# Kernel tuning notes

Measured on AMD Instinct MI355X. Metric: run time of the kernel, lower is better.

## Reference

```python
import jax, jax.numpy as jnp
import numpy as np
from jax import lax

B, CIN, COUT, H, W, K = 32, 256, 256, 56, 56, 3

def setup_inputs() -> dict:
    key = jax.random.key(0)
    k1, k2, k3 = jax.random.split(key, 3)
    inp = jax.random.normal(k1, (B, CIN, H, W), dtype=jnp.float32)
    # kaiming-style init for conv kernel, normal init for bias
    fan_in = CIN * K * K
    kernel = jax.random.normal(k2, (COUT, CIN, K, K), dtype=jnp.float32) * np.float32(np.sqrt(2.0 / fan_in))
    bias = jax.random.normal(k3, (COUT,), dtype=jnp.float32)
    return {"inp": inp, "kernel": kernel, "bias": bias}

def reference(inp, kernel, bias):
    # Equivalent to the crossbar path: im2col 3x3 patches @ stacked [kernel|bias]
    # matrix == standard conv2d(padding=1, stride=1) + bias.
    out = lax.conv_general_dilated(
        inp, kernel,
        window_strides=(1, 1),
        padding=((1, 1), (1, 1)),
        dimension_numbers=("NCHW", "OIHW", "NCHW"),
    )
    return out + bias[None, :, None, None]
```

## Files before the change

kernel.cpp:

```cpp
#include <hip/hip_runtime.h>
#include <hip/hip_bf16.h>


#define BB    32
#define CINC  256
#define COUTC 256
#define HH    56
#define WW    56
#define HP    58
#define WP    58
#define PIX_PER_IMG 3136
#define NPIX  100352
#define KTOT  2304
#define NKT   72

#define XT_BYTES ((size_t)BB*HP*WP*CINC*2)
#define AWR_FRAGS (72*16*64)
#define AWR_BYTES ((size_t)AWR_FRAGS*16)

#define BUF_SZ 8192

using frag_t = __attribute__((ext_vector_type(8))) short;
using f32x4  = __attribute__((ext_vector_type(4))) float;

__device__ __forceinline__ void gload_lds16(const void* gsrc, void* ldst) {
  __builtin_amdgcn_global_load_lds(
      (const __attribute__((address_space(1))) unsigned*)gsrc,
      (__attribute__((address_space(3))) unsigned*)ldst, 16, 0, 0);
}

__global__ void xpose_kernel(const float* __restrict__ inp,
                             __hip_bfloat16* __restrict__ xt) {
  int bid = blockIdx.x;
  int hp = bid % HP;
  int t  = bid / HP;
  int cb = t % 4;
  int b  = t / 4;
  __shared__ __hip_bfloat16 tile[64 * 60];
  int tid = threadIdx.x;
  for (int i = tid; i < 64 * 60; i += 256) tile[i] = __float2bfloat16(0.f);
  __syncthreads();
  int h = hp - 1;
  if (h >= 0 && h < HH) {
    const float* src = inp + ((size_t)(b * CINC + cb * 64) * HH + h) * WW;
    for (int i = tid; i < 64 * WW; i += 256) {
      int ci = i / WW, w = i - ci * WW;
      tile[ci * 60 + (w + 1)] = __float2bfloat16(src[(size_t)ci * HH * WW + w]);
    }
  }
  __syncthreads();
  __hip_bfloat16* dst = xt + ((size_t)(b * HP + hp) * WP) * CINC + cb * 64;
  for (int i = tid; i < WP * 64; i += 256) {
    int wp = i >> 6, ci = i & 63;
    dst[(size_t)wp * CINC + ci] = tile[ci * 60 + wp];
  }
}

__global__ void wprep_pack(const float* __restrict__ k4,
                           frag_t* __restrict__ awr) {
  int i = blockIdx.x * 256 + threadIdx.x;
  if (i >= AWR_FRAGS) return;
  int lane = i & 63;
  int mb   = (i >> 6) & 15;
  int t    = i >> 10;
  int co   = mb * 16 + (lane & 15);
  int kb   = t * 32 + (lane >> 4) * 8;
  frag_t v;
#pragma unroll
  for (int j = 0; j < 8; ++j) {
    int k = kb + j;
    int tap = k >> 8;
    int ci  = k & 255;
    __hip_bfloat16 h = __float2bfloat16(k4[(co * CINC + ci) * 9 + tap]);
    v[j] = *reinterpret_cast<short*>(&h);
  }
  awr[i] = v;
}

__global__ __launch_bounds__(256, 2) void conv_areg(
    const __hip_bfloat16* __restrict__ xt,
    const frag_t* __restrict__ awr,
    const float* __restrict__ bias,
    float* __restrict__ out) {
  __shared__ alignas(16) char lds[3 * BUF_SZ];

  const int tid  = threadIdx.x;
  const int lane = tid & 63;
  const int wid  = tid >> 6;
  const int wm   = wid >> 1;
  const int wn   = wid & 1;
  const int fr   = lane & 15;
  const int g    = lane >> 4;

  const int bid   = blockIdx.x;
  const int ntile = (bid & 7) * 98 + (bid >> 3);

  const char* xt_b = (const char*)xt;

  const int lr  = lane >> 2;
  const int sc  = ((((lane & 3) - ((lane >> 3) & 3)) & 3) << 4);

  auto mkB = [&](int jb) -> const char* {
    int px = ntile * 128 + wid * 32 + jb * 16 + lr;
    int b  = px / PIX_PER_IMG;
    int hw = px - b * PIX_PER_IMG;
    int h = hw / WW, w = hw - h * WW;
    return xt_b + (size_t)((b * HP + h) * WP + w) * (CINC * 2) + sc;
  };
  const char* pB0 = mkB(0);
  const char* pB1 = mkB(1);

#define STG(T2, WB) {                                                      \
    int _tap = (T2) >> 3; int _rr = _tap / 3, _ss = _tap - _rr * 3;        \
    size_t _bo = (size_t)(_rr * WP + _ss) * (CINC * 2)                     \
               + (size_t)((T2) & 7) * 64;                                  \
    char* _d = lds + (WB) * BUF_SZ;                                        \
    gload_lds16(pB0 + _bo, _d + wid * 2048 + 0);                           \
    gload_lds16(pB1 + _bo, _d + wid * 2048 + 1024); }

  const frag_t* abase = awr + (size_t)(wm * 8) * 64 + lane;

#define ALOAD(T1, FA) {                                                    \
    const frag_t* _p = abase + (size_t)(T1) * (16 * 64);                   \
    _Pragma("unroll") for (int m = 0; m < 8; ++m)                          \
      FA[m] = _p[m * 64]; }

  const int ckr   = (((g + (fr >> 1)) & 3) << 4);
  const int broff = (wn * 64 + fr) * 64 + ckr;

  frag_t fa0[8], fa1[8], fb[4];
  f32x4 acc[8][4] = {};

#define RSL(RB) {                                                          \
    const char* _b = lds + (RB) * BUF_SZ;                                  \
    _Pragma("unroll") for (int n = 0; n < 4; ++n)                          \
      fb[n] = *(const frag_t*)(_b + broff + n * 1024); }

#define MF(FA) {                                                           \
    __builtin_amdgcn_s_setprio(1);                                         \
    _Pragma("unroll") for (int m = 0; m < 8; ++m)                          \
    _Pragma("unroll") for (int n = 0; n < 4; ++n)                          \
      acc[m][n] = __builtin_amdgcn_mfma_f32_16x16x32_bf16(                 \
          FA[m], fb[n], acc[m][n], 0, 0, 0);                               \
    __builtin_amdgcn_s_setprio(0); }

#define BODY(T, RB, WB, FCUR, FNXT) {                                      \
    STG((T) + 2, WB);                                                      \
    ALOAD((T) + 1, FNXT);                                                  \
    RSL(RB);                                                               \
    MF(FCUR);                                                              \
    asm volatile("s_waitcnt vmcnt(10)" ::: "memory");                      \
    __builtin_amdgcn_s_barrier();                                          \
    __builtin_amdgcn_sched_barrier(0); }

  STG(0, 0);
  STG(1, 1);
  ALOAD(0, fa0);
  asm volatile("s_waitcnt vmcnt(10)" ::: "memory");
  __builtin_amdgcn_s_barrier();
  __builtin_amdgcn_sched_barrier(0);

  for (int base = 0; base < 66; base += 6) {
    BODY(base + 0, 0, 2, fa0, fa1);
    BODY(base + 1, 1, 0, fa1, fa0);
    BODY(base + 2, 2, 1, fa0, fa1);
    BODY(base + 3, 0, 2, fa1, fa0);
    BODY(base + 4, 1, 0, fa0, fa1);
    BODY(base + 5, 2, 1, fa1, fa0);
  }
  BODY(66, 0, 2, fa0, fa1);
  BODY(67, 1, 0, fa1, fa0);
  BODY(68, 2, 1, fa0, fa1);
  BODY(69, 0, 2, fa1, fa0);

  {
    ALOAD(71, fa1);
    RSL(1);
    MF(fa0);
    asm volatile("s_waitcnt vmcnt(0)" ::: "memory");
    __builtin_amdgcn_s_barrier();
    __builtin_amdgcn_sched_barrier(0);
  }
  {
    RSL(2);
    MF(fa1);
  }

  int pb[4], phw[4];
#pragma unroll
  for (int n = 0; n < 4; ++n) {
    int pxg = ntile * 128 + wn * 64 + n * 16 + fr;
    pb[n]  = pxg / PIX_PER_IMG;
    phw[n] = pxg - pb[n] * PIX_PER_IMG;
  }
#pragma unroll
  for (int m = 0; m < 8; ++m) {
#pragma unroll
    for (int rg = 0; rg < 4; ++rg) {
      int co = wm * 128 + m * 16 + g * 4 + rg;
      float bv = bias[co];
#pragma unroll
      for (int n = 0; n < 4; ++n)
        out[((size_t)pb[n] * COUTC + co) * PIX_PER_IMG + phw[n]] =
            acc[m][n][rg] + bv;
    }
  }
}

__global__ void conv_direct(const float* __restrict__ inp,
                            const float* __restrict__ kern,
                            const float* __restrict__ bias,
                            float* __restrict__ out) {
  int idx = blockIdx.x * 256 + threadIdx.x;
  if (idx >= BB * COUTC * PIX_PER_IMG) return;
  int w = idx % WW;
  int t = idx / WW;
  int h = t % HH; t /= HH;
  int co = t % COUTC;
  int b  = t / COUTC;
  float acc = bias[co];
  for (int ci = 0; ci < CINC; ++ci)
    for (int r = 0; r < 3; ++r) {
      int hh = h + r - 1;
      if (hh < 0 || hh >= HH) continue;
      for (int s = 0; s < 3; ++s) {
        int ww2 = w + s - 1;
        if (ww2 < 0 || ww2 >= WW) continue;
        acc += inp[((size_t)(b * CINC + ci) * HH + hh) * WW + ww2] *
               kern[(co * CINC + ci) * 9 + r * 3 + s];
      }
    }
  out[idx] = acc;
}

extern "C" void kernel_launch(void* const* d_in, const int* in_sizes, int n_in,
                              void* d_out, int out_size, void* d_ws, size_t ws_size,
                              hipStream_t stream) {
  const float* inp  = (const float*)d_in[0];
  const float* kern = (const float*)d_in[1];
  const float* bias = (const float*)d_in[2];
  float* out = (float*)d_out;

  size_t need = XT_BYTES + AWR_BYTES;
  if (ws_size < need) {
    int tot = BB * COUTC * PIX_PER_IMG;
    conv_direct<<<(tot + 255) / 256, 256, 0, stream>>>(inp, kern, bias, out);
    return;
  }

  __hip_bfloat16* xt = (__hip_bfloat16*)d_ws;
  frag_t* awr = (frag_t*)((char*)d_ws + XT_BYTES);

  xpose_kernel<<<BB * 4 * HP, 256, 0, stream>>>(inp, xt);
  wprep_pack<<<(AWR_FRAGS + 255) / 256, 256, 0, stream>>>(kern, awr);
  conv_areg<<<NPIX / 128, 256, 0, stream>>>(xt, awr, bias, out);
}
```

Before: 185.5 us.

## Restructure conv GEMM into 512-thread 256x256 tiles with phased ping-pong pipeline

The implicit-GEMM conv kernel now uses 512-thread blocks, each computing a 256-cout by 256-pixel tile with 8 waves in a 2x4 arrangement. This replaces 256-thread blocks at two per CU. The K loop is split into half-tile phases: staging of B into four LDS buffers, A-register prefetch and MFMA groups are interleaved with barriers and explicit waitcnts, in a ping-pong schedule. The aim is better reuse per block and more overlap of global loads with MFMA work. In exchange it runs one block per CU with many more barriers, and the tail of the loop issues redundant clamped loads.

Measured after the change: 224.4 us. 1.21x slower.

```diff
diff --git a/kernel.cpp b/kernel.cpp
--- a/kernel.cpp
+++ b/kernel.cpp
@@ -18,7 +18,8 @@
 #define AWR_FRAGS (72*16*64)
 #define AWR_BYTES ((size_t)AWR_FRAGS*16)
 
-#define BUF_SZ 8192
+#define BUF_SZ 16384
+#define NT    392
 
 using frag_t = __attribute__((ext_vector_type(8))) short;
 using f32x4  = __attribute__((ext_vector_type(4))) float;
@@ -77,119 +78,128 @@
   awr[i] = v;
 }
 
-__global__ __launch_bounds__(256, 2) void conv_areg(
+__global__ __launch_bounds__(512, 1) void conv_ph(
     const __hip_bfloat16* __restrict__ xt,
     const frag_t* __restrict__ awr,
     const float* __restrict__ bias,
     float* __restrict__ out) {
-  __shared__ alignas(16) char lds[3 * BUF_SZ];
+  __shared__ alignas(16) char lds[4 * BUF_SZ];
 
   const int tid  = threadIdx.x;
   const int lane = tid & 63;
   const int wid  = tid >> 6;
-  const int wm   = wid >> 1;
-  const int wn   = wid & 1;
+  const int wm   = wid >> 2;
+  const int wn   = wid & 3;
   const int fr   = lane & 15;
   const int g    = lane >> 4;
 
   const int bid   = blockIdx.x;
-  const int ntile = (bid & 7) * 98 + (bid >> 3);
+  const int ptile = (bid & 7) * 49 + (bid >> 3);
 
   const char* xt_b = (const char*)xt;
 
   const int lr  = lane >> 2;
   const int sc  = ((((lane & 3) - ((lane >> 3) & 3)) & 3) << 4);
 
-  auto mkB = [&](int jb) -> const char* {
-    int px = ntile * 128 + wid * 32 + jb * 16 + lr;
+  auto mkB = [&](int h) -> const char* {
+    int px = ptile * 256 + h * 128 + wid * 16 + lr;
     int b  = px / PIX_PER_IMG;
     int hw = px - b * PIX_PER_IMG;
-    int h = hw / WW, w = hw - h * WW;
-    return xt_b + (size_t)((b * HP + h) * WP + w) * (CINC * 2) + sc;
+    int hh = hw / WW, w = hw - hh * WW;
+    return xt_b + (size_t)((b * HP + hh) * WP + w) * (CINC * 2) + sc;
   };
   const char* pB0 = mkB(0);
   const char* pB1 = mkB(1);
 
-#define STG(T2, WB) {                                                      \
-    int _tap = (T2) >> 3; int _rr = _tap / 3, _ss = _tap - _rr * 3;        \
+#define STG1(KT, WB, H) {                                                  \
+    int _kt = (KT) <= 71 ? (KT) : 71;                                      \
+    int _tap = _kt >> 3; int _rr = _tap / 3, _ss = _tap - _rr * 3;         \
     size_t _bo = (size_t)(_rr * WP + _ss) * (CINC * 2)                     \
-               + (size_t)((T2) & 7) * 64;                                  \
-    char* _d = lds + (WB) * BUF_SZ;                                        \
-    gload_lds16(pB0 + _bo, _d + wid * 2048 + 0);                           \
-    gload_lds16(pB1 + _bo, _d + wid * 2048 + 1024); }
+               + (size_t)(_kt & 7) * 64;                                   \
+    gload_lds16(((H) ? pB1 : pB0) + _bo,                                   \
+                lds + (WB) * BUF_SZ + (H) * 8192 + wid * 1024); }
 
   const frag_t* abase = awr + (size_t)(wm * 8) * 64 + lane;
 
-#define ALOAD(T1, FA) {                                                    \
-    const frag_t* _p = abase + (size_t)(T1) * (16 * 64);                   \
-    _Pragma("unroll") for (int m = 0; m < 8; ++m)                          \
-      FA[m] = _p[m * 64]; }
+#define ALOAD4(T1, QM, DST) {                                              \
+    int _t = (T1) <= 71 ? (T1) : 71;                                       \
+    const frag_t* _p = abase + ((size_t)_t * 16 + (QM) * 4) * 64;          \
+    _Pragma("unroll") for (int m = 0; m < 4; ++m)                          \
+      (DST)[m] = _p[m * 64]; }
 
   const int ckr   = (((g + (fr >> 1)) & 3) << 4);
   const int broff = (wn * 64 + fr) * 64 + ckr;
 
-  frag_t fa0[8], fa1[8], fb[4];
+  frag_t fa0[8], fa1[8], fbA[4], fbB[4];
   f32x4 acc[8][4] = {};
 
-#define RSL(RB) {                                                          \
+#define RSL(RB, FB) {                                                      \
     const char* _b = lds + (RB) * BUF_SZ;                                  \
     _Pragma("unroll") for (int n = 0; n < 4; ++n)                          \
-      fb[n] = *(const frag_t*)(_b + broff + n * 1024); }
-
-#define MF(FA) {                                                           \
-    __builtin_amdgcn_s_setprio(1);                                         \
-    _Pragma("unroll") for (int m = 0; m < 8; ++m)                          \
+      (FB)[n] = *(const frag_t*)(_b + broff + n * 1024); }
+
+#define MFP(QM, FA, FB) {                                                  \
+    __builtin_amdgcn_s_setprio(1);                                        \
+    _Pragma("unroll") for (int m = 0; m < 4; ++m)                          \
     _Pragma("unroll") for (int n = 0; n < 4; ++n)                          \
-      acc[m][n] = __builtin_amdgcn_mfma_f32_16x16x32_bf16(                 \
-          FA[m], fb[n], acc[m][n], 0, 0, 0);                               \
+      acc[(QM) * 4 + m][n] = __builtin_amdgcn_mfma_f32_16x16x32_bf16(      \
+          (FA)[(QM) * 4 + m], (FB)[n], acc[(QM) * 4 + m][n], 0, 0, 0);     \
     __builtin_amdgcn_s_setprio(0); }
 
-#define BODY(T, RB, WB, FCUR, FNXT) {                                      \
-    STG((T) + 2, WB);                                                      \
-    ALOAD((T) + 1, FNXT);                                                  \
-    RSL(RB);                                                               \
-    MF(FCUR);                                                              \
-    asm volatile("s_waitcnt vmcnt(10)" ::: "memory");                      \
-    __builtin_amdgcn_s_barrier();                                          \
-    __builtin_amdgcn_sched_barrier(0); }
-
-  STG(0, 0);
-  STG(1, 1);
-  ALOAD(0, fa0);
-  asm volatile("s_waitcnt vmcnt(10)" ::: "memory");
-  __builtin_amdgcn_s_barrier();
+#define BAR()  __builtin_amdgcn_s_barrier()
+#define LGKM0() { asm volatile("s_waitcnt lgkmcnt(0)" ::: "memory");       \
+                  __builtin_amdgcn_sched_barrier(0); }
+#define VM12() { asm volatile("s_waitcnt vmcnt(12)" ::: "memory");         \
+                 __builtin_amdgcn_sched_barrier(0); }
+
+#define ITER(KT0, RB0, RB1, WB0, WB1) {                                    \
+                                         \
+    RSL(RB0, fbA);                                                         \
+    STG1((KT0) + 2, WB0, 0);                                               \
+    ALOAD4((KT0) + 1, 0, fa1);                                             \
+    BAR(); LGKM0();                                                        \
+    MFP(0, fa0, fbA);                                                      \
+    BAR();                                                                 \
+                                    \
+    STG1((KT0) + 2, WB0, 1);                                               \
+    ALOAD4((KT0) + 1, 1, fa1 + 4);                                         \
+    VM12();                                                                \
+    BAR(); LGKM0();                                                        \
+    MFP(1, fa0, fbA);                                                      \
+    BAR();                                                                 \
+                                                  \
+    RSL(RB1, fbB);                                                         \
+    STG1((KT0) + 3, WB1, 0);                                               \
+    ALOAD4((KT0) + 2, 0, fa0);                                             \
+    BAR(); LGKM0();                                                        \
+    MFP(0, fa1, fbB);                                                      \
+    BAR();                                                                 \
+                                    \
+    STG1((KT0) + 3, WB1, 1);                                               \
+    ALOAD4((KT0) + 2, 1, fa0 + 4);                                         \
+    VM12();                                                                \
+    BAR(); LGKM0();                                                        \
+    MFP(1, fa1, fbB);                                                      \
+    BAR(); }
+
+  STG1(0, 0, 0); STG1(0, 0, 1);
+  STG1(1, 1, 0); STG1(1, 1, 1);
+  ALOAD4(0, 0, fa0);
+  ALOAD4(0, 1, fa0 + 4);
+  asm volatile("s_waitcnt vmcnt(0)" ::: "memory");
+  BAR();
   __builtin_amdgcn_sched_barrier(0);
 
-  for (int base = 0; base < 66; base += 6) {
-    BODY(base + 0, 0, 2, fa0, fa1);
-    BODY(base + 1, 1, 0, fa1, fa0);
-    BODY(base + 2, 2, 1, fa0, fa1);
-    BODY(base + 3, 0, 2, fa1, fa0);
-    BODY(base + 4, 1, 0, fa0, fa1);
-    BODY(base + 5, 2, 1, fa1, fa0);
-  }
-  BODY(66, 0, 2, fa0, fa1);
-  BODY(67, 1, 0, fa1, fa0);
-  BODY(68, 2, 1, fa0, fa1);
-  BODY(69, 0, 2, fa1, fa0);
-
-  {
-    ALOAD(71, fa1);
-    RSL(1);
-    MF(fa0);
-    asm volatile("s_waitcnt vmcnt(0)" ::: "memory");
-    __builtin_amdgcn_s_barrier();
-    __builtin_amdgcn_sched_barrier(0);
-  }
-  {
-    RSL(2);
-    MF(fa1);
+  for (int b = 0; b < 18; ++b) {
+    int kt0 = b * 4;
+    ITER(kt0,     0, 1, 2, 3);
+    ITER(kt0 + 2, 2, 3, 0, 1);
   }
 
   int pb[4], phw[4];
 #pragma unroll
   for (int n = 0; n < 4; ++n) {
-    int pxg = ntile * 128 + wn * 64 + n * 16 + fr;
+    int pxg = ptile * 256 + wn * 64 + n * 16 + fr;
     pb[n]  = pxg / PIX_PER_IMG;
     phw[n] = pxg - pb[n] * PIX_PER_IMG;
   }
@@ -253,5 +263,5 @@
 
   xpose_kernel<<<BB * 4 * HP, 256, 0, stream>>>(inp, xt);
   wprep_pack<<<(AWR_FRAGS + 255) / 256, 256, 0, stream>>>(kern, awr);
-  conv_areg<<<NPIX / 128, 256, 0, stream>>>(xt, awr, bias, out);
-}
+  conv_ph<<<NT, 512, 0, stream>>>(xt, awr, bias, out);
+}
```
